# Kernel tuning notes

Measured on AMD Instinct MI355X. Metric: run time of the kernel, lower is better.

## Reference

```python
import jax, jax.numpy as jnp
import numpy as np
import math

HEAD_DIM = 128
LAMBDA_INIT = 0.8
GN_EPS = 1e-05
NEG = -1e9


def ghostmax(scores):
    # softmax with an extra implicit zero logit (softmax-plus-one)
    m = jnp.maximum(jnp.max(scores, axis=-1, keepdims=True), 0.0)
    e = jnp.exp(scores - m)
    return e / (jnp.sum(e, axis=-1, keepdims=True) + jnp.exp(-m))


def setup_inputs() -> dict:
    key = jax.random.key(0)
    ks = jax.random.split(key, 8)
    B, H2, H, S, D = 2, 16, 8, 2048, HEAD_DIM
    return {
        "q": jax.random.normal(ks[0], (B, H2, S, D), dtype=jnp.float32),
        "k": jax.random.normal(ks[1], (B, H2, S, D), dtype=jnp.float32),
        "v": jax.random.normal(ks[2], (B, H, S, D), dtype=jnp.float32),
        "lambda_q1": 0.1 * jax.random.normal(ks[3], (D,), dtype=jnp.float32),
        "lambda_k1": 0.1 * jax.random.normal(ks[4], (D,), dtype=jnp.float32),
        "lambda_q2": 0.1 * jax.random.normal(ks[5], (D,), dtype=jnp.float32),
        "lambda_k2": 0.1 * jax.random.normal(ks[6], (D,), dtype=jnp.float32),
        "gn_weight": jnp.ones((H * D,), dtype=jnp.float32),
        "gn_bias": jnp.zeros((H * D,), dtype=jnp.float32),
    }


def reference(q, k, v, lambda_q1, lambda_k1, lambda_q2, lambda_k2, gn_weight, gn_bias):
    B, H2, S, D = q.shape
    H = H2 // 2
    scaling = 1.0 / math.sqrt(D)
    # [B, 2H, S, S] attention scores
    scores = jnp.einsum("bhsd,bhtd->bhst", q, k) * scaling
    causal_mask = jnp.triu(jnp.full((S, S), NEG, dtype=scores.dtype), k=1)
    scores = scores + causal_mask[None, None]
    w = ghostmax(scores)
    w = w.reshape(B, H, 2, S, S)
    lam = (
        jnp.exp(jnp.sum(lambda_q1 * lambda_k1))
        - jnp.exp(jnp.sum(lambda_q2 * lambda_k2))
        + LAMBDA_INIT
    )
    w = w[:, :, 0] - lam * w[:, :, 1]  # [B, H, S, S]
    out = jnp.einsum("bhst,bhtd->bhsd", w, v)  # [B, H, S, D]
    # torch .reshape(B, -1, S): raw row-major reinterpretation
    out = out.reshape(B, H * D, S)
    # GroupNorm: num_groups=H over channels H*D, normalized over (group channels, seq)
    g = out.reshape(B, H, D * S)
    mean = jnp.mean(g, axis=-1, keepdims=True)
    var = jnp.var(g, axis=-1, keepdims=True)
    g = (g - mean) * jax.lax.rsqrt(var + GN_EPS)
    out = g.reshape(B, H * D, S) * gn_weight[None, :, None] + gn_bias[None, :, None]
    return out * (1.0 - LAMBDA_INIT)
```

## Files before the change

### kernel.cpp

```cpp
#include <hip/hip_runtime.h>
#include <hip/hip_bf16.h>
#include <cstddef>
#include <cstdint>


typedef __bf16 bf16x8 __attribute__((ext_vector_type(8)));
typedef __bf16 bf16x4 __attribute__((ext_vector_type(4)));
typedef float f32x4 __attribute__((ext_vector_type(4)));

constexpr int SEQ = 2048;
constexpr int DH  = 128;
constexpr int NH  = 8;
constexpr int NH2 = 16;
constexpr float SCALE  = 0.088388347648318447f;
constexpr float QSCALE = 0.127517430f;

template <bool B> struct BoolK { static constexpr bool value = B; };

constexpr size_t QK_ELEMS = (size_t)2 * NH2 * SEQ * DH;
constexpr size_t V_ELEMS  = (size_t)2 * NH  * SEQ * DH;
constexpr size_t OFF_KB   = 4096;
constexpr size_t OFF_VT   = OFF_KB + QK_ELEMS * 2;
constexpr size_t WS_NEED  = OFF_VT + V_ELEMS * 2;

__device__ __forceinline__ void load_lds16(const void* g, void* l) {
  __builtin_amdgcn_global_load_lds(
      (const __attribute__((address_space(1))) uint32_t*)g,
      (__attribute__((address_space(3))) uint32_t*)l, 16, 0, 0);
}

__device__ __forceinline__ bf16x8 cvt8(float4 a, float4 b) {
  bf16x8 r;
  r[0] = (__bf16)a.x; r[1] = (__bf16)a.y; r[2] = (__bf16)a.z; r[3] = (__bf16)a.w;
  r[4] = (__bf16)b.x; r[5] = (__bf16)b.y; r[6] = (__bf16)b.z; r[7] = (__bf16)b.w;
  return r;
}

__global__ __launch_bounds__(256) void prep_kernel(
    const float* __restrict__ k, const float* __restrict__ v,
    __bf16* __restrict__ Kb, __bf16* __restrict__ Vtb,
    float* __restrict__ stats)
{
  __shared__ float tile[32][33];
  const int id = blockIdx.x;
  if (id == 0 && threadIdx.x < 64) stats[threadIdx.x] = 0.f;
  if (id < 4096) {
    const size_t i = ((size_t)id * 256 + threadIdx.x) * 8;
    float4 a = *(const float4*)(k + i);
    float4 b = *(const float4*)(k + i + 4);
    *(bf16x8*)(Kb + i) = cvt8(a, b);
  } else {
    const int vid = id - 4096;
    const int tt = vid & 63, dt = (vid >> 6) & 3, bh = vid >> 8;
    const int tr = threadIdx.x >> 3, tc = (threadIdx.x & 7) * 4;
    const float* src = v + ((size_t)bh * SEQ + tt * 32) * DH + dt * 32;
    float4 f = *(const float4*)(src + (size_t)tr * DH + tc);
    tile[tr][tc + 0] = f.x; tile[tr][tc + 1] = f.y;
    tile[tr][tc + 2] = f.z; tile[tr][tc + 3] = f.w;
    __syncthreads();
    __bf16* dst = Vtb + ((size_t)bh * DH + dt * 32 + tr) * SEQ + tt * 32 + tc;
    bf16x4 o;
    o[0] = (__bf16)tile[tc + 0][tr];
    o[1] = (__bf16)tile[tc + 1][tr];
    o[2] = (__bf16)tile[tc + 2][tr];
    o[3] = (__bf16)tile[tc + 3][tr];
    *(bf16x4*)dst = o;
  }
}

__global__ __launch_bounds__(256, 3) void attn3_kernel(
    const float* __restrict__ Qf, const __bf16* __restrict__ Kb,
    const __bf16* __restrict__ Vtb,
    const float* __restrict__ lq1, const float* __restrict__ lk1,
    const float* __restrict__ lq2, const float* __restrict__ lk2,
    float* __restrict__ Obuf, float* __restrict__ stats)
{
  __shared__ __align__(16) __bf16 ldsK[2][2][32][128];
  __shared__ __align__(16) __bf16 ldsVt[2][128][32];
  __shared__ __align__(16) __bf16 ldsP[4][16][36];
  __shared__ float ldsLa[32];

  const int bid = (int)blockIdx.x;
  const int qt = 63 - (bid >> 4);
  const int bh = bid & 15;
  const int b = bh >> 3, h = bh & 7;
  const int tid = threadIdx.x;
  const int wv = tid >> 6;
  const int g  = wv >> 1;
  const int w2 = wv & 1;
  const int lane = tid & 63;
  const int l15 = lane & 15, quad = lane >> 4;

  float a1 = lq1[lane]*lk1[lane] + lq1[lane+64]*lk1[lane+64];
  float a2 = lq2[lane]*lk2[lane] + lq2[lane+64]*lk2[lane+64];
  #pragma unroll
  for (int off = 1; off < 64; off <<= 1) {
    a1 += __shfl_xor(a1, off);
    a2 += __shfl_xor(a2, off);
  }
  const float lam = __expf(a1) - __expf(a2) + 0.8f;

  const size_t headQK = (size_t)(b*NH2 + 2*h + g) * SEQ * DH;
  const float*  Qh  = Qf + headQK;
  const __bf16* Kh  = Kb + headQK;
  const __bf16* Vth = Vtb + (size_t)(b*NH + h) * DH * SEQ;

  size_t goffK[4];
  #pragma unroll
  for (int i = 0; i < 4; ++i) {
    const int c  = i*128 + w2*64 + lane;
    const int R  = c >> 4, cs = c & 15;
    goffK[i] = (size_t)R * DH + ((cs ^ (R & 15)) * 8);
  }
  size_t goffV[2];
  #pragma unroll
  for (int i = 0; i < 2; ++i) {
    const int c  = i*256 + tid;
    const int d  = c >> 2, cs = c & 3;
    goffV[i] = (size_t)d * SEQ + ((cs ^ (d & 3)) * 8);
  }

  __bf16* ldsKg = &ldsK[g][0][0][0];
  __bf16* ldsVb = &ldsVt[0][0][0];

  const int qb = qt * 32;
  const int nsteps = qt + 1;
  const int rbase = qb + w2*16;

  bf16x8 qf[4];
  {
    const float* src = Qh + (size_t)(rbase + l15)*DH + quad*8;
    #pragma unroll
    for (int kd = 0; kd < 4; ++kd) {
      float4 f0 = *(const float4*)(src + kd*32);
      float4 f1 = *(const float4*)(src + kd*32 + 4);
      f0.x *= QSCALE; f0.y *= QSCALE; f0.z *= QSCALE; f0.w *= QSCALE;
      f1.x *= QSCALE; f1.y *= QSCALE; f1.z *= QSCALE; f1.w *= QSCALE;
      qf[kd] = cvt8(f0, f1);
    }
  }

  f32x4 oacc[8];
  float lsum[4];
  #pragma unroll
  for (int nt = 0; nt < 8; ++nt) oacc[nt] = (f32x4){0.f,0.f,0.f,0.f};
  #pragma unroll
  for (int r = 0; r < 4; ++r) lsum[r] = 0.f;

  {
    #pragma unroll
    for (int i = 0; i < 4; ++i)
      load_lds16(Kh + goffK[i], ldsKg + i*1024 + w2*512);
    #pragma unroll
    for (int i = 0; i < 2; ++i)
      load_lds16(Vth + goffV[i], ldsVb + i*2048 + wv*512);
  }
  __syncthreads();

  for (int st = 0; st < nsteps; ++st) {
    const int cur = st & 1;
    const int kbt = st * 32;

    if (st + 1 < nsteps) {
      const int nxt = cur ^ 1;
      const __bf16* kg = Kh + (size_t)(kbt + 32) * DH;
      #pragma unroll
      for (int i = 0; i < 4; ++i)
        load_lds16(kg + goffK[i], ldsKg + nxt*4096 + i*1024 + w2*512);
      #pragma unroll
      for (int i = 0; i < 2; ++i)
        load_lds16(Vth + (kbt + 32) + goffV[i], ldsVb + nxt*4096 + i*2048 + wv*512);
    }

    f32x4 sacc[2];
    sacc[0] = (f32x4){0.f,0.f,0.f,0.f};
    sacc[1] = (f32x4){0.f,0.f,0.f,0.f};
    __builtin_amdgcn_s_setprio(1);
    #pragma unroll
    for (int n = 0; n < 2; ++n)
      #pragma unroll
      for (int kd = 0; kd < 4; ++kd) {
        bf16x8 kf = *(const bf16x8*)&ldsK[g][cur][n*16 + l15][((kd*4 + quad) ^ l15) * 8];
        sacc[n] = __builtin_amdgcn_mfma_f32_16x16x32_bf16(qf[kd], kf, sacc[n], 0, 0, 0);
      }
    __builtin_amdgcn_s_setprio(0);

    auto sm_body = [&](auto MASKC) {
      constexpr bool MASKED = decltype(MASKC)::value;
      #pragma unroll
      for (int r = 0; r < 4; ++r) {
        float p0 = __builtin_amdgcn_exp2f(sacc[0][r]);
        float p1 = __builtin_amdgcn_exp2f(sacc[1][r]);
        if constexpr (MASKED) {
          const int qr = rbase + quad*4 + r;
          if (kbt + l15      > qr) p0 = 0.f;
          if (kbt + l15 + 16 > qr) p1 = 0.f;
        }
        lsum[r] += p0 + p1;
        ldsP[wv][quad*4 + r][l15]      = (__bf16)p0;
        ldsP[wv][quad*4 + r][l15 + 16] = (__bf16)p1;
      }
    };
    if (kbt + 31 <= rbase) sm_body(BoolK<false>{});
    else                   sm_body(BoolK<true>{});

    {
      bf16x8 pf = *(const bf16x8*)&ldsP[wv][l15][quad*8];
      __builtin_amdgcn_s_setprio(1);
      #pragma unroll
      for (int nt = 0; nt < 8; ++nt) {
        bf16x8 vf = *(const bf16x8*)&ldsVt[cur][nt*16 + l15][(quad ^ (l15 & 3)) * 8];
        oacc[nt] = __builtin_amdgcn_mfma_f32_16x16x32_bf16(pf, vf, oacc[nt], 0, 0, 0);
      }
      __builtin_amdgcn_s_setprio(0);
    }
    __syncthreads();
  }

  float lr[4];
  #pragma unroll
  for (int r = 0; r < 4; ++r) {
    float vsum = lsum[r];
    #pragma unroll
    for (int off = 1; off < 16; off <<= 1) vsum += __shfl_xor(vsum, off);
    lr[r] = vsum;
  }

  float* Oscr = (float*)&ldsK[0][0][0][0];
  if (g == 1) {
    #pragma unroll
    for (int nt = 0; nt < 8; ++nt)
      #pragma unroll
      for (int r = 0; r < 4; ++r)
        Oscr[(w2*16 + quad*4 + r)*128 + nt*16 + l15] = oacc[nt][r];
    if (l15 == 0) {
      #pragma unroll
      for (int r = 0; r < 4; ++r)
        ldsLa[w2*16 + quad*4 + r] = lr[r];
    }
  }
  __syncthreads();

  if (g == 0) {
    float* obase = Obuf + (size_t)(b*NH + h) * SEQ * DH;
    float sum = 0.f, ss = 0.f;
    #pragma unroll
    for (int r = 0; r < 4; ++r) {
      const int row = w2*16 + quad*4 + r;
      const float l0 = lr[r] + 1.0f;
      const float l1 = ldsLa[row] + 1.0f;
      const float i0 = 1.0f / l0;
      const float i1 = lam / l1;
      float* orow = obase + (size_t)(qb + row) * DH + l15;
      #pragma unroll
      for (int nt = 0; nt < 8; ++nt) {
        const float o1 = Oscr[row*128 + nt*16 + l15];
        const float val = oacc[nt][r] * i0 - o1 * i1;
        orow[nt*16] = val;
        sum += val;
        ss  += val * val;
      }
    }
    #pragma unroll
    for (int off = 1; off < 64; off <<= 1) {
      sum += __shfl_xor(sum, off);
      ss  += __shfl_xor(ss, off);
    }
    if (lane == 0) {
      atomicAdd(&stats[2*(b*NH + h)],     sum);
      atomicAdd(&stats[2*(b*NH + h) + 1], ss);
    }
  }
}

__global__ __launch_bounds__(256) void attn_fb_kernel(
    const float* __restrict__ q, const float* __restrict__ k,
    const float* __restrict__ v,
    const float* __restrict__ lq1, const float* __restrict__ lk1,
    const float* __restrict__ lq2, const float* __restrict__ lk2,
    float* __restrict__ Obuf, float* __restrict__ stats)
{
  __shared__ __align__(16) __bf16 lds_k[2][32][136];
  __shared__ __align__(16) __bf16 lds_vt[128][40];
  __shared__ __align__(16) __bf16 lds_p[4][2][16][40];

  const int qt = blockIdx.x, h = blockIdx.y, b = blockIdx.z;
  const int qb = qt * 64;
  const int tid = threadIdx.x;
  const int w = tid >> 6, lane = tid & 63;
  const int l15 = lane & 15, quad = lane >> 4;

  float a1 = lq1[lane]*lk1[lane] + lq1[lane+64]*lk1[lane+64];
  float a2 = lq2[lane]*lk2[lane] + lq2[lane+64]*lk2[lane+64];
  #pragma unroll
  for (int off = 1; off < 64; off <<= 1) {
    a1 += __shfl_xor(a1, off);
    a2 += __shfl_xor(a2, off);
  }
  const float lam = __expf(a1) - __expf(a2) + 0.8f;

  const float* qh0 = q + (size_t)(b*NH2 + 2*h) * SEQ * DH;
  const float* qh1 = qh0 + (size_t)SEQ * DH;
  const float* kh0 = k + (size_t)(b*NH2 + 2*h) * SEQ * DH;
  const float* kh1 = kh0 + (size_t)SEQ * DH;
  const float* vh  = v + (size_t)(b*NH + h) * SEQ * DH;

  bf16x8 qf[2][4];
  {
    const int qrow = qb + w*16 + l15;
    #pragma unroll
    for (int sh = 0; sh < 2; ++sh) {
      const float* src = (sh ? qh1 : qh0) + (size_t)qrow * DH + quad*8;
      #pragma unroll
      for (int kd = 0; kd < 4; ++kd) {
        float4 f0 = *(const float4*)(src + kd*32);
        float4 f1 = *(const float4*)(src + kd*32 + 4);
        qf[sh][kd] = cvt8(f0, f1);
      }
    }
  }

  f32x4 oacc[2][8];
  #pragma unroll
  for (int sh = 0; sh < 2; ++sh)
    #pragma unroll
    for (int nt = 0; nt < 8; ++nt)
      oacc[sh][nt] = (f32x4){0.f,0.f,0.f,0.f};

  float mst[2][4] = {{0.f,0.f,0.f,0.f},{0.f,0.f,0.f,0.f}};
  float lst[2][4] = {{1.f,1.f,1.f,1.f},{1.f,1.f,1.f,1.f}};

  const int krow = tid >> 2, ksh = krow >> 5, kr = krow & 31;
  const int kd0 = (tid & 3) * 32;
  const float* ksrc0 = (ksh ? kh1 : kh0) + kd0;
  const int vt = tid >> 3, vd = (tid & 7) * 16;

  const int nsteps = (qb + 64) / 32;
  for (int st = 0; st < nsteps; ++st) {
    const int kbt = st * 32;
    {
      const float* sp = ksrc0 + (size_t)(kbt + kr) * DH;
      #pragma unroll
      for (int c = 0; c < 4; ++c) {
        float4 f0 = *(const float4*)(sp + c*8);
        float4 f1 = *(const float4*)(sp + c*8 + 4);
        *(bf16x8*)&lds_k[ksh][kr][kd0 + c*8] = cvt8(f0, f1);
      }
      const float* vp = vh + (size_t)(kbt + vt) * DH + vd;
      #pragma unroll
      for (int c = 0; c < 4; ++c) {
        float4 f = *(const float4*)(vp + c*4);
        lds_vt[vd + c*4 + 0][vt] = (__bf16)f.x;
        lds_vt[vd + c*4 + 1][vt] = (__bf16)f.y;
        lds_vt[vd + c*4 + 2][vt] = (__bf16)f.z;
        lds_vt[vd + c*4 + 3][vt] = (__bf16)f.w;
      }
    }
    __syncthreads();

    f32x4 sacc[2][2];
    #pragma unroll
    for (int sh = 0; sh < 2; ++sh)
      #pragma unroll
      for (int n = 0; n < 2; ++n)
        sacc[sh][n] = (f32x4){0.f,0.f,0.f,0.f};

    #pragma unroll
    for (int sh = 0; sh < 2; ++sh)
      #pragma unroll
      for (int n = 0; n < 2; ++n)
        #pragma unroll
        for (int kd = 0; kd < 4; ++kd) {
          bf16x8 bf = *(const bf16x8*)&lds_k[sh][n*16 + l15][kd*32 + quad*8];
          sacc[sh][n] = __builtin_amdgcn_mfma_f32_16x16x32_bf16(qf[sh][kd], bf, sacc[sh][n], 0, 0, 0);
        }

    const int qrow0 = qb + w*16 + quad*4;
    const int c0 = kbt + l15, c1 = c0 + 16;
    #pragma unroll
    for (int sh = 0; sh < 2; ++sh) {
      #pragma unroll
      for (int r = 0; r < 4; ++r) {
        float s0 = sacc[sh][0][r] * SCALE;
        float s1 = sacc[sh][1][r] * SCALE;
        const int qr = qrow0 + r;
        if (c0 > qr) s0 = -1e30f;
        if (c1 > qr) s1 = -1e30f;
        float mx = fmaxf(s0, s1);
        #pragma unroll
        for (int off = 1; off < 16; off <<= 1)
          mx = fmaxf(mx, __shfl_xor(mx, off));
        const float mnew = fmaxf(mst[sh][r], mx);
        const float alpha = __expf(mst[sh][r] - mnew);
        mst[sh][r] = mnew;
        const float p0 = __expf(s0 - mnew);
        const float p1 = __expf(s1 - mnew);
        float rs = p0 + p1;
        #pragma unroll
        for (int off = 1; off < 16; off <<= 1)
          rs += __shfl_xor(rs, off);
        lst[sh][r] = lst[sh][r] * alpha + rs;
        #pragma unroll
        for (int nt = 0; nt < 8; ++nt)
          oacc[sh][nt][r] *= alpha;
        lds_p[w][sh][quad*4 + r][l15]      = (__bf16)p0;
        lds_p[w][sh][quad*4 + r][l15 + 16] = (__bf16)p1;
      }
    }

    {
      bf16x8 pf0 = *(const bf16x8*)&lds_p[w][0][l15][quad*8];
      bf16x8 pf1 = *(const bf16x8*)&lds_p[w][1][l15][quad*8];
      #pragma unroll
      for (int nt = 0; nt < 8; ++nt) {
        bf16x8 vf = *(const bf16x8*)&lds_vt[nt*16 + l15][quad*8];
        oacc[0][nt] = __builtin_amdgcn_mfma_f32_16x16x32_bf16(pf0, vf, oacc[0][nt], 0, 0, 0);
        oacc[1][nt] = __builtin_amdgcn_mfma_f32_16x16x32_bf16(pf1, vf, oacc[1][nt], 0, 0, 0);
      }
    }
    __syncthreads();
  }

  const int qrow0 = qb + w*16 + quad*4;
  float* obase = Obuf + (size_t)(b*NH + h) * SEQ * DH;
  float sum = 0.f, ss = 0.f;
  #pragma unroll
  for (int r = 0; r < 4; ++r) {
    const float i0 = 1.0f / lst[0][r];
    const float i1 = lam / lst[1][r];
    float* orow = obase + (size_t)(qrow0 + r) * DH + l15;
    #pragma unroll
    for (int nt = 0; nt < 8; ++nt) {
      const float val = oacc[0][nt][r] * i0 - oacc[1][nt][r] * i1;
      orow[nt*16] = val;
      sum += val;
      ss  += val * val;
    }
  }
  #pragma unroll
  for (int off = 1; off < 64; off <<= 1) {
    sum += __shfl_xor(sum, off);
    ss  += __shfl_xor(ss, off);
  }
  if (lane == 0) {
    atomicAdd(&stats[2*(b*NH + h)],     sum);
    atomicAdd(&stats[2*(b*NH + h) + 1], ss);
  }
}

__global__ __launch_bounds__(256) void norm_kernel(
    float* __restrict__ Obuf, const float* __restrict__ stats,
    const float* __restrict__ gw, const float* __restrict__ gb)
{
  const int idx = (blockIdx.x * 256 + threadIdx.x) * 4;
  const int bh = idx >> 18;
  const int local = idx & 262143;
  const float inv = 1.0f / 262144.0f;
  const float mean = stats[2*bh] * inv;
  const float var  = stats[2*bh + 1] * inv - mean * mean;
  const float rstd = rsqrtf(var + 1e-5f);
  const int c = ((bh & 7) << 7) + (local >> 11);
  const float wq = gw[c] * rstd;
  const float bq = gb[c];
  float4 o = *(const float4*)(Obuf + idx);
  float4 r;
  r.x = ((o.x - mean) * wq + bq) * 0.2f;
  r.y = ((o.y - mean) * wq + bq) * 0.2f;
  r.z = ((o.z - mean) * wq + bq) * 0.2f;
  r.w = ((o.w - mean) * wq + bq) * 0.2f;
  *(float4*)(Obuf + idx) = r;
}

extern "C" void kernel_launch(void* const* d_in, const int* in_sizes, int n_in,
                              void* d_out, int out_size, void* d_ws, size_t ws_size,
                              hipStream_t stream) {
  const float* q   = (const float*)d_in[0];
  const float* k   = (const float*)d_in[1];
  const float* v   = (const float*)d_in[2];
  const float* lq1 = (const float*)d_in[3];
  const float* lk1 = (const float*)d_in[4];
  const float* lq2 = (const float*)d_in[5];
  const float* lk2 = (const float*)d_in[6];
  const float* gw  = (const float*)d_in[7];
  const float* gb  = (const float*)d_in[8];
  float* out = (float*)d_out;
  float* stats = (float*)d_ws;

  if (ws_size >= WS_NEED) {
    __bf16* Kb  = (__bf16*)((char*)d_ws + OFF_KB);
    __bf16* Vtb = (__bf16*)((char*)d_ws + OFF_VT);

    prep_kernel<<<8192, 256, 0, stream>>>(k, v, Kb, Vtb, stats);

    attn3_kernel<<<1024, 256, 0, stream>>>(q, Kb, Vtb,
        lq1, lk1, lq2, lk2, out, stats);
  } else {
    (void)hipMemsetAsync(d_ws, 0, 256, stream);
    attn_fb_kernel<<<dim3(32, NH, 2), 256, 0, stream>>>(q, k, v,
        lq1, lk1, lq2, lk2, out, stats);
  }

  const int total = 2 * NH * SEQ * DH;
  norm_kernel<<<total / 1024, 256, 0, stream>>>(out, stats, gw, gb);
}
```

Baseline: 211.9 us.

## Pair causal query tiles per block, triple-buffer K, read V directly

Each block now handles two query tiles, qt and 63-qt, so every block does the same amount of causal work, and the grid shrinks from 1024 to 512 blocks. K staging in LDS becomes a triple-buffered ring with explicit vmcnt waits and raw barriers. The V^T tile is loaded straight from global memory into registers instead of being staged through LDS. The block now holds two sets of accumulators, which raises register pressure (launch bounds drop from 3 to 2 blocks per CU), and the global V reads add latency.

Measured after the change: 273.9 us. 1.29x slower.

```diff
diff --git a/kernel.cpp b/kernel.cpp
--- a/kernel.cpp
+++ b/kernel.cpp
@@ -68,21 +68,21 @@
   }
 }
 
-__global__ __launch_bounds__(256, 3) void attn3_kernel(
+__global__ __launch_bounds__(256, 2) void attn3_kernel(
     const float* __restrict__ Qf, const __bf16* __restrict__ Kb,
     const __bf16* __restrict__ Vtb,
     const float* __restrict__ lq1, const float* __restrict__ lk1,
     const float* __restrict__ lq2, const float* __restrict__ lk2,
     float* __restrict__ Obuf, float* __restrict__ stats)
 {
-  __shared__ __align__(16) __bf16 ldsK[2][2][32][128];
-  __shared__ __align__(16) __bf16 ldsVt[2][128][32];
+  __shared__ __align__(16) __bf16 ldsK[2][3][32][128];
   __shared__ __align__(16) __bf16 ldsP[4][16][36];
   __shared__ float ldsLa[32];
 
   const int bid = (int)blockIdx.x;
-  const int qt = 63 - (bid >> 4);
+  const int pair = bid >> 4;
   const int bh = bid & 15;
+  const int qtA = pair, qtB = 63 - pair;
   const int b = bh >> 3, h = bh & 7;
   const int tid = threadIdx.x;
   const int wv = tid >> 6;
@@ -104,74 +104,80 @@
   const float*  Qh  = Qf + headQK;
   const __bf16* Kh  = Kb + headQK;
   const __bf16* Vth = Vtb + (size_t)(b*NH + h) * DH * SEQ;
-
-  size_t goffK[4];
+  const __bf16* Vlane = Vth + (size_t)l15 * SEQ + quad*8;
+
+  int goffK[4];
   #pragma unroll
   for (int i = 0; i < 4; ++i) {
     const int c  = i*128 + w2*64 + lane;
     const int R  = c >> 4, cs = c & 15;
-    goffK[i] = (size_t)R * DH + ((cs ^ (R & 15)) * 8);
-  }
-  size_t goffV[2];
-  #pragma unroll
-  for (int i = 0; i < 2; ++i) {
-    const int c  = i*256 + tid;
-    const int d  = c >> 2, cs = c & 3;
-    goffV[i] = (size_t)d * SEQ + ((cs ^ (d & 3)) * 8);
-  }
-
+    goffK[i] = R * DH + ((cs ^ (R & 15)) * 8);
+  }
   __bf16* ldsKg = &ldsK[g][0][0][0];
-  __bf16* ldsVb = &ldsVt[0][0][0];
-
-  const int qb = qt * 32;
-  const int nsteps = qt + 1;
-  const int rbase = qb + w2*16;
-
-  bf16x8 qf[4];
+
+  const int nA = qtA + 1;
+  const int total = nA + qtB + 1;
+  const int rbA = qtA*32 + w2*16;
+  const int rbB = qtB*32 + w2*16;
+
+  bf16x8 qfA[4], qfB[4];
   {
-    const float* src = Qh + (size_t)(rbase + l15)*DH + quad*8;
+    const float* srcA = Qh + (size_t)(rbA + l15)*DH + quad*8;
+    const float* srcB = Qh + (size_t)(rbB + l15)*DH + quad*8;
     #pragma unroll
     for (int kd = 0; kd < 4; ++kd) {
-      float4 f0 = *(const float4*)(src + kd*32);
-      float4 f1 = *(const float4*)(src + kd*32 + 4);
+      float4 f0 = *(const float4*)(srcA + kd*32);
+      float4 f1 = *(const float4*)(srcA + kd*32 + 4);
       f0.x *= QSCALE; f0.y *= QSCALE; f0.z *= QSCALE; f0.w *= QSCALE;
       f1.x *= QSCALE; f1.y *= QSCALE; f1.z *= QSCALE; f1.w *= QSCALE;
-      qf[kd] = cvt8(f0, f1);
-    }
-  }
-
-  f32x4 oacc[8];
-  float lsum[4];
-  #pragma unroll
-  for (int nt = 0; nt < 8; ++nt) oacc[nt] = (f32x4){0.f,0.f,0.f,0.f};
-  #pragma unroll
-  for (int r = 0; r < 4; ++r) lsum[r] = 0.f;
-
-  {
+      qfA[kd] = cvt8(f0, f1);
+      float4 g0 = *(const float4*)(srcB + kd*32);
+      float4 g1 = *(const float4*)(srcB + kd*32 + 4);
+      g0.x *= QSCALE; g0.y *= QSCALE; g0.z *= QSCALE; g0.w *= QSCALE;
+      g1.x *= QSCALE; g1.y *= QSCALE; g1.z *= QSCALE; g1.w *= QSCALE;
+      qfB[kd] = cvt8(g0, g1);
+    }
+  }
+
+  f32x4 oaccA[8], oaccB[8];
+  float lsA[4] = {0.f,0.f,0.f,0.f}, lsB[4] = {0.f,0.f,0.f,0.f};
+  #pragma unroll
+  for (int nt = 0; nt < 8; ++nt) {
+    oaccA[nt] = (f32x4){0.f,0.f,0.f,0.f};
+    oaccB[nt] = (f32x4){0.f,0.f,0.f,0.f};
+  }
+
+  auto stageK = [&](int f) {
+    const int kb = (f < nA ? f : f - nA) * 32;
+    const int slot = f % 3;
+    const __bf16* src = Kh + (size_t)kb * DH;
+    __bf16* dst = ldsKg + slot*4096;
     #pragma unroll
     for (int i = 0; i < 4; ++i)
-      load_lds16(Kh + goffK[i], ldsKg + i*1024 + w2*512);
-    #pragma unroll
-    for (int i = 0; i < 2; ++i)
-      load_lds16(Vth + goffV[i], ldsVb + i*2048 + wv*512);
-  }
-  __syncthreads();
-
-  for (int st = 0; st < nsteps; ++st) {
-    const int cur = st & 1;
-    const int kbt = st * 32;
-
-    if (st + 1 < nsteps) {
-      const int nxt = cur ^ 1;
-      const __bf16* kg = Kh + (size_t)(kbt + 32) * DH;
-      #pragma unroll
-      for (int i = 0; i < 4; ++i)
-        load_lds16(kg + goffK[i], ldsKg + nxt*4096 + i*1024 + w2*512);
-      #pragma unroll
-      for (int i = 0; i < 2; ++i)
-        load_lds16(Vth + (kbt + 32) + goffV[i], ldsVb + nxt*4096 + i*2048 + wv*512);
-    }
-
+      load_lds16(src + goffK[i], dst + i*1024 + w2*512);
+  };
+
+  auto sm_body = [&](const f32x4& s0, const f32x4& s1, float (&ls)[4],
+                     const int rb, const int kbt, auto MASKC) {
+    constexpr bool MASKED = decltype(MASKC)::value;
+    #pragma unroll
+    for (int r = 0; r < 4; ++r) {
+      float p0 = __builtin_amdgcn_exp2f(s0[r]);
+      float p1 = __builtin_amdgcn_exp2f(s1[r]);
+      if constexpr (MASKED) {
+        const int qr = rb + quad*4 + r;
+        if (kbt + l15      > qr) p0 = 0.f;
+        if (kbt + l15 + 16 > qr) p1 = 0.f;
+      }
+      ls[r] += p0 + p1;
+      ldsP[wv][quad*4 + r][l15]      = (__bf16)p0;
+      ldsP[wv][quad*4 + r][l15 + 16] = (__bf16)p1;
+    }
+  };
+
+  auto step_body = [&](bf16x8 (&qf)[4], f32x4 (&oacc)[8], float (&ls)[4],
+                       const int rb, const bool diag, const int kbt,
+                       const int slot, bf16x8 (&vf)[8]) {
     f32x4 sacc[2];
     sacc[0] = (f32x4){0.f,0.f,0.f,0.f};
     sacc[1] = (f32x4){0.f,0.f,0.f,0.f};
@@ -180,96 +186,114 @@
     for (int n = 0; n < 2; ++n)
       #pragma unroll
       for (int kd = 0; kd < 4; ++kd) {
-        bf16x8 kf = *(const bf16x8*)&ldsK[g][cur][n*16 + l15][((kd*4 + quad) ^ l15) * 8];
+        bf16x8 kf = *(const bf16x8*)&ldsK[g][slot][n*16 + l15][((kd*4 + quad) ^ l15) * 8];
         sacc[n] = __builtin_amdgcn_mfma_f32_16x16x32_bf16(qf[kd], kf, sacc[n], 0, 0, 0);
       }
     __builtin_amdgcn_s_setprio(0);
 
-    auto sm_body = [&](auto MASKC) {
-      constexpr bool MASKED = decltype(MASKC)::value;
+    if (diag) sm_body(sacc[0], sacc[1], ls, rb, kbt, BoolK<true>{});
+    else      sm_body(sacc[0], sacc[1], ls, rb, kbt, BoolK<false>{});
+
+    bf16x8 pf = *(const bf16x8*)&ldsP[wv][l15][quad*8];
+    __builtin_amdgcn_s_setprio(1);
+    #pragma unroll
+    for (int nt = 0; nt < 8; ++nt)
+      oacc[nt] = __builtin_amdgcn_mfma_f32_16x16x32_bf16(pf, vf[nt], oacc[nt], 0, 0, 0);
+    __builtin_amdgcn_s_setprio(0);
+  };
+
+  stageK(0);
+  stageK(1);
+  asm volatile("s_waitcnt vmcnt(4)" ::: "memory");
+  __builtin_amdgcn_sched_barrier(0);
+  __builtin_amdgcn_s_barrier();
+  __builtin_amdgcn_sched_barrier(0);
+
+  for (int f = 0; f < total; ++f) {
+    const int slot = f % 3;
+    const bool isA = f < nA;
+    const int kbt = (isA ? f : f - nA) * 32;
+    const bool more = (f + 2) < total;
+
+    bf16x8 vf[8];
+    #pragma unroll
+    for (int nt = 0; nt < 8; ++nt)
+      vf[nt] = *(const bf16x8*)(Vlane + (size_t)nt*16*SEQ + kbt);
+    __builtin_amdgcn_sched_barrier(0);
+
+    if (more) stageK(f + 2);
+    __builtin_amdgcn_sched_barrier(0);
+
+    if (isA) step_body(qfA, oaccA, lsA, rbA, f == qtA,      kbt, slot, vf);
+    else     step_body(qfB, oaccB, lsB, rbB, f == total - 1, kbt, slot, vf);
+
+    if (more) { asm volatile("s_waitcnt vmcnt(4)" ::: "memory"); }
+    else      { asm volatile("s_waitcnt vmcnt(0)" ::: "memory"); }
+    __builtin_amdgcn_sched_barrier(0);
+    __builtin_amdgcn_s_barrier();
+    __builtin_amdgcn_sched_barrier(0);
+  }
+
+  float osum = 0.f, oss = 0.f;
+  float* Oscr = (float*)&ldsK[0][0][0][0];
+  float* obase = Obuf + (size_t)(b*NH + h) * SEQ * DH;
+
+  auto epi = [&](f32x4 (&oacc)[8], float (&ls)[4], const int qt) {
+    float lr[4];
+    #pragma unroll
+    for (int r = 0; r < 4; ++r) {
+      float v = ls[r];
+      #pragma unroll
+      for (int off = 1; off < 16; off <<= 1) v += __shfl_xor(v, off);
+      lr[r] = v;
+    }
+    __builtin_amdgcn_s_barrier();
+    if (g == 1) {
+      #pragma unroll
+      for (int nt = 0; nt < 8; ++nt)
+        #pragma unroll
+        for (int r = 0; r < 4; ++r)
+          Oscr[(w2*16 + quad*4 + r)*128 + nt*16 + l15] = oacc[nt][r];
+      if (l15 == 0) {
+        #pragma unroll
+        for (int r = 0; r < 4; ++r)
+          ldsLa[w2*16 + quad*4 + r] = lr[r];
+      }
+    }
+    asm volatile("s_waitcnt lgkmcnt(0)" ::: "memory");
+    __builtin_amdgcn_s_barrier();
+    if (g == 0) {
       #pragma unroll
       for (int r = 0; r < 4; ++r) {
-        float p0 = __builtin_amdgcn_exp2f(sacc[0][r]);
-        float p1 = __builtin_amdgcn_exp2f(sacc[1][r]);
-        if constexpr (MASKED) {
-          const int qr = rbase + quad*4 + r;
-          if (kbt + l15      > qr) p0 = 0.f;
-          if (kbt + l15 + 16 > qr) p1 = 0.f;
+        const int row = w2*16 + quad*4 + r;
+        const float l0 = lr[r] + 1.0f;
+        const float l1 = ldsLa[row] + 1.0f;
+        const float i0 = 1.0f / l0;
+        const float i1 = lam / l1;
+        float* orow = obase + (size_t)(qt*32 + row) * DH + l15;
+        #pragma unroll
+        for (int nt = 0; nt < 8; ++nt) {
+          const float o1 = Oscr[row*128 + nt*16 + l15];
+          const float val = oacc[nt][r] * i0 - o1 * i1;
+          orow[nt*16] = val;
+          osum += val;
+          oss  += val * val;
         }
-        lsum[r] += p0 + p1;
-        ldsP[wv][quad*4 + r][l15]      = (__bf16)p0;
-        ldsP[wv][quad*4 + r][l15 + 16] = (__bf16)p1;
-      }
-    };
-    if (kbt + 31 <= rbase) sm_body(BoolK<false>{});
-    else                   sm_body(BoolK<true>{});
-
-    {
-      bf16x8 pf = *(const bf16x8*)&ldsP[wv][l15][quad*8];
-      __builtin_amdgcn_s_setprio(1);
-      #pragma unroll
-      for (int nt = 0; nt < 8; ++nt) {
-        bf16x8 vf = *(const bf16x8*)&ldsVt[cur][nt*16 + l15][(quad ^ (l15 & 3)) * 8];
-        oacc[nt] = __builtin_amdgcn_mfma_f32_16x16x32_bf16(pf, vf, oacc[nt], 0, 0, 0);
-      }
-      __builtin_amdgcn_s_setprio(0);
-    }
-    __syncthreads();
-  }
-
-  float lr[4];
-  #pragma unroll
-  for (int r = 0; r < 4; ++r) {
-    float vsum = lsum[r];
-    #pragma unroll
-    for (int off = 1; off < 16; off <<= 1) vsum += __shfl_xor(vsum, off);
-    lr[r] = vsum;
-  }
-
-  float* Oscr = (float*)&ldsK[0][0][0][0];
-  if (g == 1) {
-    #pragma unroll
-    for (int nt = 0; nt < 8; ++nt)
-      #pragma unroll
-      for (int r = 0; r < 4; ++r)
-        Oscr[(w2*16 + quad*4 + r)*128 + nt*16 + l15] = oacc[nt][r];
-    if (l15 == 0) {
-      #pragma unroll
-      for (int r = 0; r < 4; ++r)
-        ldsLa[w2*16 + quad*4 + r] = lr[r];
-    }
-  }
-  __syncthreads();
-
-  if (g == 0) {
-    float* obase = Obuf + (size_t)(b*NH + h) * SEQ * DH;
-    float sum = 0.f, ss = 0.f;
-    #pragma unroll
-    for (int r = 0; r < 4; ++r) {
-      const int row = w2*16 + quad*4 + r;
-      const float l0 = lr[r] + 1.0f;
-      const float l1 = ldsLa[row] + 1.0f;
-      const float i0 = 1.0f / l0;
-      const float i1 = lam / l1;
-      float* orow = obase + (size_t)(qb + row) * DH + l15;
-      #pragma unroll
-      for (int nt = 0; nt < 8; ++nt) {
-        const float o1 = Oscr[row*128 + nt*16 + l15];
-        const float val = oacc[nt][r] * i0 - o1 * i1;
-        orow[nt*16] = val;
-        sum += val;
-        ss  += val * val;
-      }
-    }
-    #pragma unroll
-    for (int off = 1; off < 64; off <<= 1) {
-      sum += __shfl_xor(sum, off);
-      ss  += __shfl_xor(ss, off);
-    }
-    if (lane == 0) {
-      atomicAdd(&stats[2*(b*NH + h)],     sum);
-      atomicAdd(&stats[2*(b*NH + h) + 1], ss);
-    }
+      }
+    }
+  };
+
+  epi(oaccA, lsA, qtA);
+  epi(oaccB, lsB, qtB);
+
+  #pragma unroll
+  for (int off = 1; off < 64; off <<= 1) {
+    osum += __shfl_xor(osum, off);
+    oss  += __shfl_xor(oss, off);
+  }
+  if (g == 0 && lane == 0) {
+    atomicAdd(&stats[2*(b*NH + h)],     osum);
+    atomicAdd(&stats[2*(b*NH + h) + 1], oss);
   }
 }
 
@@ -492,7 +516,7 @@
 
     prep_kernel<<<8192, 256, 0, stream>>>(k, v, Kb, Vtb, stats);
 
-    attn3_kernel<<<1024, 256, 0, stream>>>(q, Kb, Vtb,
+    attn3_kernel<<<512, 256, 0, stream>>>(q, Kb, Vtb,
         lq1, lk1, lq2, lk2, out, stats);
   } else {
     (void)hipMemsetAsync(d_ws, 0, 256, stream);
```

## Pair short and long causal query tiles per block for balanced work

Applied to the files above, without the earlier changes.

Each block now processes two query tiles, qt and 63-qt, so every block does the same total number of causal KV steps, and the grid is halved to 512 blocks. The first K/V tile of the second pass is prefetched during the last step of the first pass. Oscr moves into its own LDS array so it no longer aliases the K buffers that hold that prefetched tile, and launch bounds drop to 2 blocks per SM. This removes tail imbalance from causal triangles but lowers occupancy and adds LDS use, and only 512 blocks remain to spread across the GPU.

Measured after the change: 208.7 us. Within noise of the previous version (-1.5%).

```diff
diff --git a/kernel.cpp b/kernel.cpp
--- a/kernel.cpp
+++ b/kernel.cpp
@@ -68,7 +68,7 @@
   }
 }
 
-__global__ __launch_bounds__(256, 3) void attn3_kernel(
+__global__ __launch_bounds__(256, 2) void attn3_kernel(
     const float* __restrict__ Qf, const __bf16* __restrict__ Kb,
     const __bf16* __restrict__ Vtb,
     const float* __restrict__ lq1, const float* __restrict__ lk1,
@@ -78,10 +78,11 @@
   __shared__ __align__(16) __bf16 ldsK[2][2][32][128];
   __shared__ __align__(16) __bf16 ldsVt[2][128][32];
   __shared__ __align__(16) __bf16 ldsP[4][16][36];
+  __shared__ __align__(16) float  Oscr[32 * 128];
   __shared__ float ldsLa[32];
 
   const int bid = (int)blockIdx.x;
-  const int qt = 63 - (bid >> 4);
+  const int pair = bid >> 4;
   const int bh = bid & 15;
   const int b = bh >> 3, h = bh & 7;
   const int tid = threadIdx.x;
@@ -123,153 +124,156 @@
   __bf16* ldsKg = &ldsK[g][0][0][0];
   __bf16* ldsVb = &ldsVt[0][0][0];
 
-  const int qb = qt * 32;
-  const int nsteps = qt + 1;
-  const int rbase = qb + w2*16;
-
-  bf16x8 qf[4];
-  {
-    const float* src = Qh + (size_t)(rbase + l15)*DH + quad*8;
-    #pragma unroll
-    for (int kd = 0; kd < 4; ++kd) {
-      float4 f0 = *(const float4*)(src + kd*32);
-      float4 f1 = *(const float4*)(src + kd*32 + 4);
-      f0.x *= QSCALE; f0.y *= QSCALE; f0.z *= QSCALE; f0.w *= QSCALE;
-      f1.x *= QSCALE; f1.y *= QSCALE; f1.z *= QSCALE; f1.w *= QSCALE;
-      qf[kd] = cvt8(f0, f1);
-    }
-  }
-
-  f32x4 oacc[8];
-  float lsum[4];
-  #pragma unroll
-  for (int nt = 0; nt < 8; ++nt) oacc[nt] = (f32x4){0.f,0.f,0.f,0.f};
-  #pragma unroll
-  for (int r = 0; r < 4; ++r) lsum[r] = 0.f;
-
-  {
+  auto stage = [&](int kb, int buf) {
+    const __bf16* kg = Kh + (size_t)kb * DH;
     #pragma unroll
     for (int i = 0; i < 4; ++i)
-      load_lds16(Kh + goffK[i], ldsKg + i*1024 + w2*512);
+      load_lds16(kg + goffK[i], ldsKg + buf*4096 + i*1024 + w2*512);
     #pragma unroll
     for (int i = 0; i < 2; ++i)
-      load_lds16(Vth + goffV[i], ldsVb + i*2048 + wv*512);
-  }
-  __syncthreads();
-
-  for (int st = 0; st < nsteps; ++st) {
-    const int cur = st & 1;
-    const int kbt = st * 32;
-
-    if (st + 1 < nsteps) {
-      const int nxt = cur ^ 1;
-      const __bf16* kg = Kh + (size_t)(kbt + 32) * DH;
-      #pragma unroll
-      for (int i = 0; i < 4; ++i)
-        load_lds16(kg + goffK[i], ldsKg + nxt*4096 + i*1024 + w2*512);
-      #pragma unroll
-      for (int i = 0; i < 2; ++i)
-        load_lds16(Vth + (kbt + 32) + goffV[i], ldsVb + nxt*4096 + i*2048 + wv*512);
-    }
-
-    f32x4 sacc[2];
-    sacc[0] = (f32x4){0.f,0.f,0.f,0.f};
-    sacc[1] = (f32x4){0.f,0.f,0.f,0.f};
-    __builtin_amdgcn_s_setprio(1);
-    #pragma unroll
-    for (int n = 0; n < 2; ++n)
+      load_lds16(Vth + kb + goffV[i], ldsVb + buf*4096 + i*2048 + wv*512);
+  };
+
+  float osum = 0.f, oss = 0.f;
+  float* obase = Obuf + (size_t)(b*NH + h) * SEQ * DH;
+
+  int buf = 0;
+  stage(0, 0);
+
+  const int qtA = pair, qtB = 63 - pair;
+
+  for (int t = 0; t < 2; ++t) {
+    const int qt = t ? qtB : qtA;
+    const int nsteps = qt + 1;
+    const int rbase = qt*32 + w2*16;
+
+    bf16x8 qf[4];
+    {
+      const float* src = Qh + (size_t)(rbase + l15)*DH + quad*8;
       #pragma unroll
       for (int kd = 0; kd < 4; ++kd) {
-        bf16x8 kf = *(const bf16x8*)&ldsK[g][cur][n*16 + l15][((kd*4 + quad) ^ l15) * 8];
-        sacc[n] = __builtin_amdgcn_mfma_f32_16x16x32_bf16(qf[kd], kf, sacc[n], 0, 0, 0);
-      }
-    __builtin_amdgcn_s_setprio(0);
-
-    auto sm_body = [&](auto MASKC) {
-      constexpr bool MASKED = decltype(MASKC)::value;
+        float4 f0 = *(const float4*)(src + kd*32);
+        float4 f1 = *(const float4*)(src + kd*32 + 4);
+        f0.x *= QSCALE; f0.y *= QSCALE; f0.z *= QSCALE; f0.w *= QSCALE;
+        f1.x *= QSCALE; f1.y *= QSCALE; f1.z *= QSCALE; f1.w *= QSCALE;
+        qf[kd] = cvt8(f0, f1);
+      }
+    }
+
+    f32x4 oacc[8];
+    float lsum[4];
+    #pragma unroll
+    for (int nt = 0; nt < 8; ++nt) oacc[nt] = (f32x4){0.f,0.f,0.f,0.f};
+    #pragma unroll
+    for (int r = 0; r < 4; ++r) lsum[r] = 0.f;
+
+    if (t == 0) __syncthreads();
+
+    for (int st = 0; st < nsteps; ++st) {
+      const int kbt = st * 32;
+
+      if (st + 1 < nsteps)      stage(kbt + 32, buf ^ 1);
+      else if (t == 0)          stage(0,        buf ^ 1);
+
+      f32x4 sacc[2];
+      sacc[0] = (f32x4){0.f,0.f,0.f,0.f};
+      sacc[1] = (f32x4){0.f,0.f,0.f,0.f};
+      __builtin_amdgcn_s_setprio(1);
+      #pragma unroll
+      for (int n = 0; n < 2; ++n)
+        #pragma unroll
+        for (int kd = 0; kd < 4; ++kd) {
+          bf16x8 kf = *(const bf16x8*)&ldsK[g][buf][n*16 + l15][((kd*4 + quad) ^ l15) * 8];
+          sacc[n] = __builtin_amdgcn_mfma_f32_16x16x32_bf16(qf[kd], kf, sacc[n], 0, 0, 0);
+        }
+      __builtin_amdgcn_s_setprio(0);
+
+      auto sm_body = [&](auto MASKC) {
+        constexpr bool MASKED = decltype(MASKC)::value;
+        #pragma unroll
+        for (int r = 0; r < 4; ++r) {
+          float p0 = __builtin_amdgcn_exp2f(sacc[0][r]);
+          float p1 = __builtin_amdgcn_exp2f(sacc[1][r]);
+          if constexpr (MASKED) {
+            const int qr = rbase + quad*4 + r;
+            if (kbt + l15      > qr) p0 = 0.f;
+            if (kbt + l15 + 16 > qr) p1 = 0.f;
+          }
+          lsum[r] += p0 + p1;
+          ldsP[wv][quad*4 + r][l15]      = (__bf16)p0;
+          ldsP[wv][quad*4 + r][l15 + 16] = (__bf16)p1;
+        }
+      };
+      if (kbt + 31 <= rbase) sm_body(BoolK<false>{});
+      else                   sm_body(BoolK<true>{});
+
+      {
+        bf16x8 pf = *(const bf16x8*)&ldsP[wv][l15][quad*8];
+        __builtin_amdgcn_s_setprio(1);
+        #pragma unroll
+        for (int nt = 0; nt < 8; ++nt) {
+          bf16x8 vf = *(const bf16x8*)&ldsVt[buf][nt*16 + l15][(quad ^ (l15 & 3)) * 8];
+          oacc[nt] = __builtin_amdgcn_mfma_f32_16x16x32_bf16(pf, vf, oacc[nt], 0, 0, 0);
+        }
+        __builtin_amdgcn_s_setprio(0);
+      }
+      __syncthreads();
+      buf ^= 1;
+    }
+
+    float lr[4];
+    #pragma unroll
+    for (int r = 0; r < 4; ++r) {
+      float v = lsum[r];
+      #pragma unroll
+      for (int off = 1; off < 16; off <<= 1) v += __shfl_xor(v, off);
+      lr[r] = v;
+    }
+
+    if (g == 1) {
+      #pragma unroll
+      for (int nt = 0; nt < 8; ++nt)
+        #pragma unroll
+        for (int r = 0; r < 4; ++r)
+          Oscr[(w2*16 + quad*4 + r)*128 + nt*16 + l15] = oacc[nt][r];
+      if (l15 == 0) {
+        #pragma unroll
+        for (int r = 0; r < 4; ++r)
+          ldsLa[w2*16 + quad*4 + r] = lr[r];
+      }
+    }
+    __syncthreads();
+
+    if (g == 0) {
       #pragma unroll
       for (int r = 0; r < 4; ++r) {
-        float p0 = __builtin_amdgcn_exp2f(sacc[0][r]);
-        float p1 = __builtin_amdgcn_exp2f(sacc[1][r]);
-        if constexpr (MASKED) {
-          const int qr = rbase + quad*4 + r;
-          if (kbt + l15      > qr) p0 = 0.f;
-          if (kbt + l15 + 16 > qr) p1 = 0.f;
+        const int row = w2*16 + quad*4 + r;
+        const float l0 = lr[r] + 1.0f;
+        const float l1 = ldsLa[row] + 1.0f;
+        const float i0 = 1.0f / l0;
+        const float i1 = lam / l1;
+        float* orow = obase + (size_t)(qt*32 + row) * DH + l15;
+        #pragma unroll
+        for (int nt = 0; nt < 8; ++nt) {
+          const float o1 = Oscr[row*128 + nt*16 + l15];
+          const float val = oacc[nt][r] * i0 - o1 * i1;
+          orow[nt*16] = val;
+          osum += val;
+          oss  += val * val;
         }
-        lsum[r] += p0 + p1;
-        ldsP[wv][quad*4 + r][l15]      = (__bf16)p0;
-        ldsP[wv][quad*4 + r][l15 + 16] = (__bf16)p1;
-      }
-    };
-    if (kbt + 31 <= rbase) sm_body(BoolK<false>{});
-    else                   sm_body(BoolK<true>{});
-
-    {
-      bf16x8 pf = *(const bf16x8*)&ldsP[wv][l15][quad*8];
-      __builtin_amdgcn_s_setprio(1);
-      #pragma unroll
-      for (int nt = 0; nt < 8; ++nt) {
-        bf16x8 vf = *(const bf16x8*)&ldsVt[cur][nt*16 + l15][(quad ^ (l15 & 3)) * 8];
-        oacc[nt] = __builtin_amdgcn_mfma_f32_16x16x32_bf16(pf, vf, oacc[nt], 0, 0, 0);
-      }
-      __builtin_amdgcn_s_setprio(0);
+      }
     }
     __syncthreads();
   }
 
-  float lr[4];
-  #pragma unroll
-  for (int r = 0; r < 4; ++r) {
-    float vsum = lsum[r];
-    #pragma unroll
-    for (int off = 1; off < 16; off <<= 1) vsum += __shfl_xor(vsum, off);
-    lr[r] = vsum;
-  }
-
-  float* Oscr = (float*)&ldsK[0][0][0][0];
-  if (g == 1) {
-    #pragma unroll
-    for (int nt = 0; nt < 8; ++nt)
-      #pragma unroll
-      for (int r = 0; r < 4; ++r)
-        Oscr[(w2*16 + quad*4 + r)*128 + nt*16 + l15] = oacc[nt][r];
-    if (l15 == 0) {
-      #pragma unroll
-      for (int r = 0; r < 4; ++r)
-        ldsLa[w2*16 + quad*4 + r] = lr[r];
-    }
-  }
-  __syncthreads();
-
-  if (g == 0) {
-    float* obase = Obuf + (size_t)(b*NH + h) * SEQ * DH;
-    float sum = 0.f, ss = 0.f;
-    #pragma unroll
-    for (int r = 0; r < 4; ++r) {
-      const int row = w2*16 + quad*4 + r;
-      const float l0 = lr[r] + 1.0f;
-      const float l1 = ldsLa[row] + 1.0f;
-      const float i0 = 1.0f / l0;
-      const float i1 = lam / l1;
-      float* orow = obase + (size_t)(qb + row) * DH + l15;
-      #pragma unroll
-      for (int nt = 0; nt < 8; ++nt) {
-        const float o1 = Oscr[row*128 + nt*16 + l15];
-        const float val = oacc[nt][r] * i0 - o1 * i1;
-        orow[nt*16] = val;
-        sum += val;
-        ss  += val * val;
-      }
-    }
-    #pragma unroll
-    for (int off = 1; off < 64; off <<= 1) {
-      sum += __shfl_xor(sum, off);
-      ss  += __shfl_xor(ss, off);
-    }
-    if (lane == 0) {
-      atomicAdd(&stats[2*(b*NH + h)],     sum);
-      atomicAdd(&stats[2*(b*NH + h) + 1], ss);
-    }
+  #pragma unroll
+  for (int off = 1; off < 64; off <<= 1) {
+    osum += __shfl_xor(osum, off);
+    oss  += __shfl_xor(oss, off);
+  }
+  if (g == 0 && lane == 0) {
+    atomicAdd(&stats[2*(b*NH + h)],     osum);
+    atomicAdd(&stats[2*(b*NH + h) + 1], oss);
   }
 }
 
@@ -492,7 +496,7 @@
 
     prep_kernel<<<8192, 256, 0, stream>>>(k, v, Kb, Vtb, stats);
 
-    attn3_kernel<<<1024, 256, 0, stream>>>(q, Kb, Vtb,
+    attn3_kernel<<<512, 256, 0, stream>>>(q, Kb, Vtb,
         lq1, lk1, lq2, lk2, out, stats);
   } else {
     (void)hipMemsetAsync(d_ws, 0, 256, stream);
```
